# Kernel optimization log

Hardware: AMD Instinct MI355X
Metric: run time of the kernel (lower is better)

## Reference

```python
import jax, jax.numpy as jnp
import numpy as np
import math

B, L, D, H, FF = 2, 2048, 1024, 16, 4096
FACTOR = 5
EPS = 1e-5


def _ln(x, g, b):
    mu = jnp.mean(x, axis=-1, keepdims=True)
    var = jnp.mean((x - mu) ** 2, axis=-1, keepdims=True)
    return (x - mu) * jax.lax.rsqrt(var + EPS) * g + b


def setup_inputs() -> dict:
    key = jax.random.key(0)
    ks = jax.random.split(key, 16)
    s = D ** -0.5
    sample_k = min(FACTOR * int(np.ceil(np.log(L))), L)  # 40
    return {
        "x": jax.random.normal(ks[0], (B, L, D), jnp.float32),
        "Wq": jax.random.normal(ks[1], (D, D), jnp.float32) * s,
        "bq": jnp.zeros((D,), jnp.float32),
        "Wk": jax.random.normal(ks[2], (D, D), jnp.float32) * s,
        "bk": jnp.zeros((D,), jnp.float32),
        "Wv": jax.random.normal(ks[3], (D, D), jnp.float32) * s,
        "bv": jnp.zeros((D,), jnp.float32),
        "Wo": jax.random.normal(ks[4], (D, D), jnp.float32) * s,
        "bo": jnp.zeros((D,), jnp.float32),
        "ln1_g": jnp.ones((D,), jnp.float32),
        "ln1_b": jnp.zeros((D,), jnp.float32),
        "W1": jax.random.normal(ks[5], (D, FF), jnp.float32) * s,
        "b1": jnp.zeros((FF,), jnp.float32),
        "W2": jax.random.normal(ks[6], (FF, D), jnp.float32) * (FF ** -0.5),
        "b2": jnp.zeros((D,), jnp.float32),
        "ln2_g": jnp.ones((D,), jnp.float32),
        "ln2_b": jnp.zeros((D,), jnp.float32),
        "index_sample": jax.random.randint(ks[7], (L, sample_k), 0, L),
    }


def _prob_attn(Q, K, V, index_sample):
    # Q,K,V: [B,H,L,Dh]; Informer ProbAttention with mask_flag=True (causal).
    b, h, l, dh = Q.shape
    n_top = min(FACTOR * int(np.ceil(np.log(l))), l)
    # sampled scores: Q[l] . K[index_sample[l, s]]
    K_s = K[:, :, index_sample]                                  # [B,H,L,S,Dh]
    QKs = jnp.einsum("bhld,bhlsd->bhls", Q, K_s)                 # [B,H,L,S]
    M = QKs.max(-1) - QKs.sum(-1) / l                             # sparsity measure
    _, M_top = jax.lax.top_k(M, n_top)                            # [B,H,u]
    Q_red = jnp.take_along_axis(Q, M_top[..., None], axis=2)      # [B,H,u,Dh]
    scale = 1.0 / jnp.sqrt(jnp.asarray(dh, jnp.float32))
    scores = jnp.einsum("bhud,bhld->bhul", Q_red, K) * scale      # [B,H,u,L]
    causal = jnp.arange(l)[None, None, None, :] > M_top[..., None]
    scores = jnp.where(causal, -jnp.inf, scores)
    attn = jax.nn.softmax(scores, axis=-1)
    upd = jnp.einsum("bhul,bhld->bhud", attn, V)                  # [B,H,u,Dh]
    # initial context for masked case: running cumsum of V
    context = jnp.cumsum(V, axis=2)
    bi = jnp.arange(b)[:, None, None]
    hi = jnp.arange(h)[None, :, None]
    context = context.at[bi, hi, M_top].set(upd)
    return context                                               # [B,H,L,Dh]


def reference(x, Wq, bq, Wk, bk, Wv, bv, Wo, bo, ln1_g, ln1_b,
              W1, b1, W2, b2, ln2_g, ln2_b, index_sample):
    b, l, d = x.shape
    dh = d // H
    Q = (x @ Wq + bq).reshape(b, l, H, dh).transpose(0, 2, 1, 3)
    K = (x @ Wk + bk).reshape(b, l, H, dh).transpose(0, 2, 1, 3)
    V = (x @ Wv + bv).reshape(b, l, H, dh).transpose(0, 2, 1, 3)
    ctx = _prob_attn(Q, K, V, index_sample)
    ctx = ctx.transpose(0, 2, 1, 3).reshape(b, l, d)
    attn_out = ctx @ Wo + bo
    x1 = _ln(x + attn_out, ln1_g, ln1_b)
    ff = jnp.maximum(x1 @ W1 + b1, 0.0) @ W2 + b2
    return _ln(x1 + ff, ln2_g, ln2_b)
```

## Files before the change

### kernel.cpp

```cpp
#include <hip/hip_runtime.h>
#include <hip/hip_bf16.h>
#include <hip/hip_fp16.h>
#include <math.h>

constexpr int B = 2, L = 2048, D = 1024, H = 16, DH = 64, FFD = 4096;
constexpr int S = 40;
constexpr int U = 40;
constexpr float EPS = 1e-5f;
constexpr int NCHUNK = 32;
constexpr int CHLEN = L / NCHUNK;
constexpr int LD3 = 3 * D;
constexpr int LD2 = 2 * D;
constexpr int LDA2 = 2 * D;
constexpr int JT = 128;
constexpr int NJC = L / JT;

typedef __attribute__((ext_vector_type(8))) short short8;
typedef __attribute__((ext_vector_type(8))) _Float16 half8;
typedef __attribute__((ext_vector_type(4))) float f32x4;

__device__ __forceinline__ unsigned short f2bf(float v) {
  __hip_bfloat16 h = __float2bfloat16(v);
  return __builtin_bit_cast(unsigned short, h);
}
__device__ __forceinline__ float bf2f(unsigned short u) {
  unsigned int x = ((unsigned int)u) << 16;
  return __builtin_bit_cast(float, x);
}
__device__ __forceinline__ unsigned short f2h(float v) {
  __half h = __float2half(v);
  return __builtin_bit_cast(unsigned short, h);
}
__device__ __forceinline__ float h2f(unsigned short u) {
  return __half2float(__builtin_bit_cast(__half, u));
}

__device__ __forceinline__ void gload16(const void* g, void* l) {
  __builtin_amdgcn_global_load_lds(
      (const __attribute__((address_space(1))) void*)g,
      (__attribute__((address_space(3))) void*)l, 16, 0, 0);
}

template<int GBN, int MINB, bool RELU, bool OUT_BF16, bool F16, bool DUPA>
__global__ __launch_bounds__(256, MINB) void gemm_kernel(
    const unsigned short* __restrict__ A,
    const unsigned short* __restrict__ Bt,
    const float* __restrict__ bias,
    const float* __restrict__ biasB,
    void* __restrict__ C, int M, int N, int K, int KA) {
  constexpr int GBM = 128, GBK = 64;
  constexpr int ABUF = GBM * GBK;
  constexpr int BBUF = GBN * GBK;
  constexpr int BUFS = ABUF + BBUF;
  constexpr int NI = GBN / 32;
  constexpr int NLOADS = 4 + GBN / 32;
  __shared__ short lds[2 * BUFS];

  const int tid  = threadIdx.x;
  const int lane = tid & 63;
  const int wid  = tid >> 6;
  const int wr = wid >> 1;
  const int wc = wid & 1;

  const int nwg  = gridDim.x * gridDim.y;
  const int orig = blockIdx.y * gridDim.x + blockIdx.x;
  const int wg   = (orig & 7) * (nwg >> 3) + (orig >> 3);
  const int bm = (wg / gridDim.x) * GBM;
  const int bn = (wg % gridDim.x) * GBN;

  const int srow  = lane >> 3;
  const int sslot = (lane & 7) ^ srow;
  const unsigned short* aS = A  + (size_t)(bm + wid * 8 + srow) * KA + sslot * 8;
  const unsigned short* bS = Bt + (size_t)(bn + wid * 8 + srow) * K  + sslot * 8;
  short* la0 = lds + wid * 8 * GBK;
  short* lb0 = lds + ABUF + wid * 8 * GBK;

  auto STAGE = [&](int buf, int kt) {
    const int akt = (DUPA && kt >= 16) ? kt - 16 : kt;
    const unsigned short* ap = aS + (size_t)akt * GBK;
    const unsigned short* bp = bS + (size_t)kt  * GBK;
    short* la = la0 + buf * BUFS;
    short* lb = lb0 + buf * BUFS;
    gload16(ap,                   la);
    gload16(ap + (size_t)32 * KA, la + 32 * GBK);
    gload16(ap + (size_t)64 * KA, la + 64 * GBK);
    gload16(ap + (size_t)96 * KA, la + 96 * GBK);
    #pragma unroll
    for (int r = 0; r < GBN / 32; ++r)
      gload16(bp + (size_t)(r * 32) * K, lb + r * 32 * GBK);
  };

  const int fr = lane & 15, g = lane >> 4;
  const int nt = K / GBK;

  STAGE(0, 0);

  f32x4 acc[4][NI] = {};
  int cur = 0;
  for (int t = 0; t < nt; ++t) {
    const int kt = (t + 1 < nt) ? t + 1 : t;
    STAGE(cur ^ 1, kt);
    if constexpr (NLOADS == 8)
      asm volatile("s_waitcnt vmcnt(8)" ::: "memory");
    else
      asm volatile("s_waitcnt vmcnt(6)" ::: "memory");
    __builtin_amdgcn_sched_barrier(0);
    __builtin_amdgcn_s_barrier();

    const short* la = lds + cur * BUFS;
    const short* lb = la + ABUF;
    short8 av[2][4], bv[2][NI];
    #pragma unroll
    for (int kk = 0; kk < 2; ++kk) {
      #pragma unroll
      for (int mi = 0; mi < 4; ++mi) {
        const int row = wr * 64 + mi * 16 + fr;
        av[kk][mi] = *(const short8*)&la[row * GBK + ((((kk << 2) | g) ^ (fr & 7)) << 3)];
      }
      #pragma unroll
      for (int ni = 0; ni < NI; ++ni) {
        const int row = wc * (GBN / 2) + ni * 16 + fr;
        bv[kk][ni] = *(const short8*)&lb[row * GBK + ((((kk << 2) | g) ^ (fr & 7)) << 3)];
      }
    }
    __builtin_amdgcn_s_setprio(1);
    #pragma unroll
    for (int kk = 0; kk < 2; ++kk)
      #pragma unroll
      for (int mi = 0; mi < 4; ++mi)
        #pragma unroll
        for (int ni = 0; ni < NI; ++ni) {
          if constexpr (F16)
            acc[mi][ni] = __builtin_amdgcn_mfma_f32_16x16x32_f16(
                __builtin_bit_cast(half8, av[kk][mi]),
                __builtin_bit_cast(half8, bv[kk][ni]), acc[mi][ni], 0, 0, 0);
          else
            acc[mi][ni] = __builtin_amdgcn_mfma_f32_16x16x32_bf16(
                av[kk][mi], bv[kk][ni], acc[mi][ni], 0, 0, 0);
        }
    __builtin_amdgcn_s_setprio(0);
    asm volatile("s_waitcnt lgkmcnt(0)" ::: "memory");
    __builtin_amdgcn_sched_barrier(0);
    __builtin_amdgcn_s_barrier();
    cur ^= 1;
  }

  #pragma unroll
  for (int ni = 0; ni < NI; ++ni) {
    const int col = bn + wc * (GBN / 2) + ni * 16 + fr;
    const float bcol = DUPA ? (col < D ? bias[col] : biasB[col - D]) : bias[col];
    #pragma unroll
    for (int mi = 0; mi < 4; ++mi) {
      #pragma unroll
      for (int j = 0; j < 4; ++j) {
        const int rowg = bm + wr * 64 + mi * 16 + (g << 2) + j;
        float v = acc[mi][ni][j] + bcol;
        if (RELU) v = fmaxf(v, 0.f);
        if (OUT_BF16) ((unsigned short*)C)[(size_t)rowg * N + col] = f2bf(v);
        else          ((float*)C)[(size_t)rowg * N + col] = v;
      }
    }
  }
}

__global__ __launch_bounds__(512, 1) void gemm_ff1_8ph_kernel(
    const unsigned short* __restrict__ A,
    const unsigned short* __restrict__ Bt,
    const float* __restrict__ bias,
    unsigned short* __restrict__ C, int M, int N, int K) {
  constexpr int BK = 64;
  __shared__ short lds8[2 * 32768];

  const int tid  = threadIdx.x;
  const int lane = tid & 63;
  const int wid  = tid >> 6;
  const int wrm  = wid >> 2;
  const int wcn  = wid & 3;

  const int nwg  = gridDim.x * gridDim.y;
  const int orig = blockIdx.y * gridDim.x + blockIdx.x;
  const int wg   = (orig & 7) * (nwg >> 3) + (orig >> 3);
  const int bm = (wg / gridDim.x) * 256;
  const int bn = (wg % gridDim.x) * 256;

  const int srow  = lane >> 3;
  const int sslot = (lane & 7) ^ srow;
  const unsigned short* aS = A  + (size_t)(bm + wid * 8 + srow) * K + sslot * 8;
  const unsigned short* bS = Bt + (size_t)(bn + wid * 8 + srow) * K + sslot * 8;
  short* ldsA0 = lds8 + wid * 8 * BK;
  short* ldsB0 = lds8 + 16384 + wid * 8 * BK;

  auto STAGE2 = [&](int buf, int kt, int part) {
    if (part < 2) {
      const unsigned short* ap = aS + (size_t)kt * BK;
      short* la = ldsA0 + buf * 32768;
      const int r0 = part * 128;
      gload16(ap + (size_t)r0 * K,        la + r0 * BK);
      gload16(ap + (size_t)(r0 + 64) * K, la + (r0 + 64) * BK);
    } else {
      const unsigned short* bp = bS + (size_t)kt * BK;
      short* lb = ldsB0 + buf * 32768;
      const int r0 = (part - 2) * 128;
      gload16(bp + (size_t)r0 * K,        lb + r0 * BK);
      gload16(bp + (size_t)(r0 + 64) * K, lb + (r0 + 64) * BK);
    }
  };

  const int fr = lane & 15, g = lane >> 4;
  const int nt = K / BK;

  #pragma unroll
  for (int p = 0; p < 4; ++p) STAGE2(0, 0, p);

  f32x4 acc[8][4] = {};
  short8 av[2][4], bv0[2][2], bv1[2][2];
  int bc = 0;
  for (int t = 0; t < nt; ++t) {
    const int kt = (t + 1 < nt) ? t + 1 : t;
    const short* la = lds8 + bc * 32768;
    const short* lb = la + 16384;

    STAGE2(bc ^ 1, kt, 0);
    asm volatile("s_waitcnt vmcnt(2)" ::: "memory");
    __builtin_amdgcn_sched_barrier(0);
    __builtin_amdgcn_s_barrier();

    #pragma unroll
    for (int kk = 0; kk < 2; ++kk) {
      #pragma unroll
      for (int mi = 0; mi < 4; ++mi) {
        const int row = wrm * 128 + mi * 16 + fr;
        av[kk][mi] = *(const short8*)&la[row * BK + ((((kk << 2) | g) ^ (fr & 7)) << 3)];
      }
      #pragma unroll
      for (int ni = 0; ni < 2; ++ni) {
        const int row = wcn * 64 + ni * 16 + fr;
        bv0[kk][ni] = *(const short8*)&lb[row * BK + ((((kk << 2) | g) ^ (fr & 7)) << 3)];
      }
    }
    asm volatile("s_waitcnt lgkmcnt(0)" ::: "memory");
    __builtin_amdgcn_sched_barrier(0);
    __builtin_amdgcn_s_setprio(1);
    #pragma unroll
    for (int kk = 0; kk < 2; ++kk)
      #pragma unroll
      for (int mi = 0; mi < 4; ++mi)
        #pragma unroll
        for (int ni = 0; ni < 2; ++ni)
          acc[mi][ni] = __builtin_amdgcn_mfma_f32_16x16x32_bf16(
              av[kk][mi], bv0[kk][ni], acc[mi][ni], 0, 0, 0);
    __builtin_amdgcn_s_setprio(0);

    STAGE2(bc ^ 1, kt, 1);
    #pragma unroll
    for (int kk = 0; kk < 2; ++kk)
      #pragma unroll
      for (int ni = 0; ni < 2; ++ni) {
        const int row = wcn * 64 + 32 + ni * 16 + fr;
        bv1[kk][ni] = *(const short8*)&lb[row * BK + ((((kk << 2) | g) ^ (fr & 7)) << 3)];
      }
    asm volatile("s_waitcnt lgkmcnt(0)" ::: "memory");
    __builtin_amdgcn_sched_barrier(0);
    __builtin_amdgcn_s_setprio(1);
    #pragma unroll
    for (int kk = 0; kk < 2; ++kk)
      #pragma unroll
      for (int mi = 0; mi < 4; ++mi)
        #pragma unroll
        for (int ni = 0; ni < 2; ++ni)
          acc[mi][2 + ni] = __builtin_amdgcn_mfma_f32_16x16x32_bf16(
              av[kk][mi], bv1[kk][ni], acc[mi][2 + ni], 0, 0, 0);
    __builtin_amdgcn_s_setprio(0);

    STAGE2(bc ^ 1, kt, 2);
    #pragma unroll
    for (int kk = 0; kk < 2; ++kk)
      #pragma unroll
      for (int mi = 0; mi < 4; ++mi) {
        const int row = wrm * 128 + 64 + mi * 16 + fr;
        av[kk][mi] = *(const short8*)&la[row * BK + ((((kk << 2) | g) ^ (fr & 7)) << 3)];
      }
    asm volatile("s_waitcnt lgkmcnt(0)" ::: "memory");
    __builtin_amdgcn_sched_barrier(0);
    __builtin_amdgcn_s_setprio(1);
    #pragma unroll
    for (int kk = 0; kk < 2; ++kk)
      #pragma unroll
      for (int mi = 0; mi < 4; ++mi)
        #pragma unroll
        for (int ni = 0; ni < 2; ++ni)
          acc[4 + mi][ni] = __builtin_amdgcn_mfma_f32_16x16x32_bf16(
              av[kk][mi], bv0[kk][ni], acc[4 + mi][ni], 0, 0, 0);
    __builtin_amdgcn_s_setprio(0);

    STAGE2(bc ^ 1, kt, 3);
    __builtin_amdgcn_s_setprio(1);
    #pragma unroll
    for (int kk = 0; kk < 2; ++kk)
      #pragma unroll
      for (int mi = 0; mi < 4; ++mi)
        #pragma unroll
        for (int ni = 0; ni < 2; ++ni)
          acc[4 + mi][2 + ni] = __builtin_amdgcn_mfma_f32_16x16x32_bf16(
              av[kk][mi], bv1[kk][ni], acc[4 + mi][2 + ni], 0, 0, 0);
    __builtin_amdgcn_s_setprio(0);
    __builtin_amdgcn_s_barrier();
    bc ^= 1;
  }

  #pragma unroll
  for (int NJ = 0; NJ < 4; ++NJ) {
    const int col = bn + wcn * 64 + NJ * 16 + fr;
    const float bcol = bias[col];
    #pragma unroll
    for (int MI = 0; MI < 8; ++MI) {
      #pragma unroll
      for (int j = 0; j < 4; ++j) {
        const int rowg = bm + wrm * 128 + MI * 16 + (g << 2) + j;
        float v = fmaxf(acc[MI][NJ][j] + bcol, 0.f);
        C[(size_t)rowg * N + col] = f2bf(v);
      }
    }
  }
}

__global__ __launch_bounds__(256) void prep_kernel(
    const float* __restrict__ x, unsigned short* __restrict__ A2,
    unsigned short* __restrict__ xb,
    const float* __restrict__ Wq, const float* __restrict__ Wk,
    unsigned short* __restrict__ B2r,
    const float* __restrict__ Wv, const float* __restrict__ Wo,
    const float* __restrict__ W1, const float* __restrict__ W2,
    unsigned short* __restrict__ Wvt, unsigned short* __restrict__ Wot,
    unsigned short* __restrict__ W1t, unsigned short* __restrict__ W2t) {
  const int bid = blockIdx.x;
  __shared__ float tile[32][33];
  if (bid < 4096) {
    const int i = (bid * 256 + threadIdx.x) * 4;
    const int m = i / D, k = i % D;
    const float4 v = *(const float4*)(x + i);
    ushort4 hi, lo, bb;
    hi.x = f2h(v.x); lo.x = f2h(v.x - h2f(hi.x)); bb.x = f2bf(v.x);
    hi.y = f2h(v.y); lo.y = f2h(v.y - h2f(hi.y)); bb.y = f2bf(v.y);
    hi.z = f2h(v.z); lo.z = f2h(v.z - h2f(hi.z)); bb.z = f2bf(v.z);
    hi.w = f2h(v.w); lo.w = f2h(v.w - h2f(hi.w)); bb.w = f2bf(v.w);
    unsigned short* row = A2 + (size_t)m * LDA2;
    *(ushort4*)(row + k)     = hi;
    *(ushort4*)(row + D + k) = lo;
    *(ushort4*)(xb + i) = bb;
    return;
  }
  const int tx = threadIdx.x & 31, ty = threadIdx.x >> 5;
  if (bid < 6144) {
    const int t = bid - 4096;
    const int z = t >> 10;
    const float* W = z ? Wk : Wq;
    unsigned short* outb = B2r + (size_t)z * D * LD3;
    const int bx = ((t & 1023) & 31) * 32;
    const int by = ((t & 1023) >> 5) * 32;
    #pragma unroll
    for (int i = ty; i < 32; i += 8)
      tile[i][tx] = W[(size_t)(by + i) * D + bx + tx];
    __syncthreads();
    #pragma unroll
    for (int i = ty; i < 32; i += 8) {
      const float v = tile[tx][i];
      const unsigned short hi = f2h(v);
      const unsigned short lo = f2h(v - h2f(hi));
      unsigned short* r = outb + (size_t)(bx + i) * LD3 + (by + tx);
      r[0]     = hi;
      r[D]     = lo;
      r[2 * D] = hi;
    }
    return;
  }
  const int tb = bid - 6144;
  const float* W; unsigned short* Wt; int K, N, t;
  if (tb < 1024)      { W = Wv; Wt = Wvt; K = D;   N = D;   t = tb; }
  else if (tb < 2048) { W = Wo; Wt = Wot; K = D;   N = D;   t = tb - 1024; }
  else if (tb < 6144) { W = W1; Wt = W1t; K = D;   N = FFD; t = tb - 2048; }
  else                { W = W2; Wt = W2t; K = FFD; N = D;   t = tb - 6144; }
  const int nx = N / 32;
  const int bx = (t % nx) * 32;
  const int by = (t / nx) * 32;
  #pragma unroll
  for (int i = ty; i < 32; i += 8)
    tile[i][tx] = W[(size_t)(by + i) * N + bx + tx];
  __syncthreads();
  #pragma unroll
  for (int i = ty; i < 32; i += 8)
    Wt[(size_t)(bx + i) * K + by + tx] = f2bf(tile[tx][i]);
}

__global__ __launch_bounds__(256) void prob_m_kernel(
    const float* __restrict__ QK, const int* __restrict__ idx,
    float* __restrict__ M_) {
  const int combo = blockIdx.x;
  const int b = combo >> 2, hg = combo & 3;
  const int l = blockIdx.y;
  const int tid = threadIdx.x;
  const int wave = tid >> 6;
  const int lane = tid & 63;
  const int h = hg * 4 + wave;
  __shared__ int sidx[S];
  if (tid < S) sidx[tid] = idx[l * S + tid];
  __syncthreads();
  const int dsub = (lane & 15) * 4;
  const int sgrp = lane >> 4;
  const float4 q = *(const float4*)(QK + ((size_t)b * L + l) * LD2 + h * DH + dsub);
  float mx = -INFINITY, sm = 0.f;
  for (int s = sgrp; s < S; s += 4) {
    const float4 kv = *(const float4*)(QK + ((size_t)b * L + sidx[s]) * LD2 + D + h * DH + dsub);
    float p = q.x*kv.x + q.y*kv.y + q.z*kv.z + q.w*kv.w;
    p += __shfl_xor(p, 1);
    p += __shfl_xor(p, 2);
    p += __shfl_xor(p, 4);
    p += __shfl_xor(p, 8);
    mx = fmaxf(mx, p);
    sm += p;
  }
  mx = fmaxf(mx, __shfl_xor(mx, 16));
  mx = fmaxf(mx, __shfl_xor(mx, 32));
  sm += __shfl_xor(sm, 16);
  sm += __shfl_xor(sm, 32);
  if (lane == 0)
    M_[((size_t)b * H + h) * L + l] = mx - sm / (float)L;
}

__global__ __launch_bounds__(64) void topk_kernel(
    const float* __restrict__ M_, int* __restrict__ Mtop) {
  const int bh = blockIdx.x;
  const float* row = M_ + (size_t)bh * L;
  const int lane = threadIdx.x;
  float v[32];
  #pragma unroll
  for (int k = 0; k < 32; ++k) v[k] = row[k * 64 + lane];
  for (int u = 0; u < U; ++u) {
    float best = v[0]; int bk = 0;
    #pragma unroll
    for (int k = 1; k < 32; ++k)
      if (v[k] > best) { best = v[k]; bk = k; }
    int bidx = bk * 64 + lane;
    #pragma unroll
    for (int off = 1; off < 64; off <<= 1) {
      const float ov = __shfl_xor(best, off);
      const int   oi = __shfl_xor(bidx, off);
      if (ov > best || (ov == best && oi < bidx)) { best = ov; bidx = oi; }
    }
    if (lane == 0) Mtop[bh * U + u] = bidx;
    if ((bidx & 63) == lane) {
      const int kk = bidx >> 6;
      #pragma unroll
      for (int k = 0; k < 32; ++k) if (k == kk) v[k] = -INFINITY;
    }
  }
}

__global__ __launch_bounds__(320) void attn_p1_kernel(
    const float* __restrict__ QK, const unsigned short* __restrict__ V16,
    const int* __restrict__ Mtop,
    float* __restrict__ pmax, float* __restrict__ psum, float* __restrict__ pv) {
  const int jc = blockIdx.x, h = blockIdx.y, b = blockIdx.z;
  const int bh = b * H + h;
  const int tid = threadIdx.x;
  const int j0 = jc * JT;
  __shared__ float Qs[U][68];
  __shared__ float KVs[JT][68];
  __shared__ unsigned short ws[U][JT];

  for (int i = tid; i < U * 16; i += 320) {
    const int u = i >> 4, dq = (i & 15) << 2;
    const int row = Mtop[bh * U + u];
    *(float4*)&Qs[u][dq] =
        *(const float4*)(QK + ((size_t)b * L + row) * LD2 + h * DH + dq);
  }
  for (int i = tid; i < JT * 16; i += 320) {
    const int j = i >> 4, dq = (i & 15) << 2;
    *(float4*)&KVs[j][dq] =
        *(const float4*)(QK + ((size_t)b * L + j0 + j) * LD2 + D + h * DH + dq);
  }
  __syncthreads();

  const int u = tid >> 3, jg = tid & 7;
  const int mt = Mtop[bh * U + u];
  float sc[16];
  #pragma unroll
  for (int jt = 0; jt < 16; ++jt) sc[jt] = 0.f;
  for (int dq = 0; dq < 64; dq += 4) {
    const float4 q = *(const float4*)&Qs[u][dq];
    #pragma unroll
    for (int jt = 0; jt < 16; ++jt) {
      const float4 k = *(const float4*)&KVs[jt * 8 + jg][dq];
      sc[jt] += q.x*k.x + q.y*k.y + q.z*k.z + q.w*k.w;
    }
  }
  float m = -INFINITY;
  #pragma unroll
  for (int jt = 0; jt < 16; ++jt) {
    const int j = j0 + jt * 8 + jg;
    sc[jt] = (j <= mt) ? sc[jt] * 0.125f : -INFINITY;
    m = fmaxf(m, sc[jt]);
  }
  m = fmaxf(m, __shfl_xor(m, 1));
  m = fmaxf(m, __shfl_xor(m, 2));
  m = fmaxf(m, __shfl_xor(m, 4));
  float sum = 0.f;
  #pragma unroll
  for (int jt = 0; jt < 16; ++jt) {
    const float e = (sc[jt] == -INFINITY) ? 0.f : expf(sc[jt] - m);
    sum += e;
    ws[u][jt * 8 + jg] = f2bf(e);
  }
  sum += __shfl_xor(sum, 1);
  sum += __shfl_xor(sum, 2);
  sum += __shfl_xor(sum, 4);
  if (jg == 0) {
    pmax[(size_t)(bh * NJC + jc) * U + u] = m;
    psum[(size_t)(bh * NJC + jc) * U + u] = sum;
  }
  __syncthreads();
  for (int i = tid; i < JT * 8; i += 320) {
    const int j = i >> 3, d8 = (i & 7) << 3;
    short8 vv = *(const short8*)(V16 + ((size_t)b * L + j0 + j) * D + h * DH + d8);
    #pragma unroll
    for (int e = 0; e < 8; ++e)
      KVs[j][d8 + e] = bf2f((unsigned short)vv[e]);
  }
  __syncthreads();
  const int d = tid & 63, ug = tid >> 6;
  float acc[8] = {};
  for (int j = 0; j < JT; j += 2) {
    const float v0 = KVs[j][d], v1 = KVs[j + 1][d];
    #pragma unroll
    for (int k = 0; k < 8; ++k) {
      const int uu = ug + k * 5;
      const unsigned int wp = *(const unsigned int*)&ws[uu][j];
      acc[k] = fmaf(bf2f((unsigned short)(wp & 0xffff)), v0, acc[k]);
      acc[k] = fmaf(bf2f((unsigned short)(wp >> 16)), v1, acc[k]);
    }
  }
  #pragma unroll
  for (int k = 0; k < 8; ++k) {
    const int uu = ug + k * 5;
    pv[((size_t)(bh * NJC + jc) * U + uu) * DH + d] = acc[k];
  }
}

__global__ __launch_bounds__(64) void attn_p2_kernel(
    const float* __restrict__ pmax, const float* __restrict__ psum,
    const float* __restrict__ pv, const int* __restrict__ Mtop,
    unsigned short* __restrict__ ctx16) {
  const int bid = blockIdx.x;
  const int u = bid % U, bh = bid / U;
  const int d = threadIdx.x;
  float gmax = -INFINITY;
  for (int c = 0; c < NJC; ++c)
    gmax = fmaxf(gmax, pmax[(size_t)(bh * NJC + c) * U + u]);
  float den = 0.f, num = 0.f;
  for (int c = 0; c < NJC; ++c) {
    const float m = pmax[(size_t)(bh * NJC + c) * U + u];
    if (m == -INFINITY) continue;
    const float s = expf(m - gmax);
    den += psum[(size_t)(bh * NJC + c) * U + u] * s;
    num += pv[((size_t)(bh * NJC + c) * U + u) * DH + d] * s;
  }
  const int h = bh % H, b = bh / H;
  const int l = Mtop[bh * U + u];
  ctx16[((size_t)b * L + l) * D + h * DH + d] = f2bf(num / den);
}

__global__ __launch_bounds__(256) void cumsum_pass1(
    const unsigned short* __restrict__ V16, float* __restrict__ csums) {
  const int cp = blockIdx.x * 256 + threadIdx.x;
  const int ch = blockIdx.y, b = blockIdx.z;
  size_t base = ((size_t)b * L + (size_t)ch * CHLEN) * D + cp * 2;
  float a0 = 0.f, a1 = 0.f;
  for (int i = 0; i < CHLEN; ++i) {
    const unsigned int u = *(const unsigned int*)(V16 + base + (size_t)i * D);
    a0 += bf2f((unsigned short)(u & 0xffff));
    a1 += bf2f((unsigned short)(u >> 16));
  }
  float* cs = csums + ((size_t)b * NCHUNK + ch) * D + cp * 2;
  cs[0] = a0; cs[1] = a1;
}

__global__ __launch_bounds__(256) void cumsum_pass2(
    const unsigned short* __restrict__ V16, const float* __restrict__ csums,
    unsigned short* __restrict__ ctx16) {
  const int cp = blockIdx.x * 256 + threadIdx.x;
  const int ch = blockIdx.y, b = blockIdx.z;
  float a0 = 0.f, a1 = 0.f;
  for (int j = 0; j < ch; ++j) {
    const float* cs = csums + ((size_t)b * NCHUNK + j) * D + cp * 2;
    a0 += cs[0]; a1 += cs[1];
  }
  size_t base = ((size_t)b * L + (size_t)ch * CHLEN) * D + cp * 2;
  for (int i = 0; i < CHLEN; ++i) {
    const size_t o = base + (size_t)i * D;
    const unsigned int u = *(const unsigned int*)(V16 + o);
    a0 += bf2f((unsigned short)(u & 0xffff));
    a1 += bf2f((unsigned short)(u >> 16));
    *(unsigned int*)(ctx16 + o) =
        (unsigned int)f2bf(a0) | ((unsigned int)f2bf(a1) << 16);
  }
}

template<bool ABF16>
__global__ __launch_bounds__(256) void add_ln_kernel(
    const void* __restrict__ a_, const unsigned short* __restrict__ r,
    const float* __restrict__ g, const float* __restrict__ be,
    float* __restrict__ out, unsigned short* __restrict__ out16) {
  const int row  = blockIdx.x * 4 + (threadIdx.x >> 6);
  const int lane = threadIdx.x & 63;
  float v[16];
  float s = 0.f;
  #pragma unroll
  for (int j = 0; j < 4; ++j) {
    const int c = j * 256 + lane * 4;
    float4 av;
    if (ABF16) {
      ushort4 ua = *(const ushort4*)((const unsigned short*)a_ + (size_t)row * D + c);
      av.x = bf2f(ua.x); av.y = bf2f(ua.y); av.z = bf2f(ua.z); av.w = bf2f(ua.w);
    } else {
      av = *(const float4*)((const float*)a_ + (size_t)row * D + c);
    }
    const ushort4 ur = *(const ushort4*)(r + (size_t)row * D + c);
    v[j*4+0] = av.x + bf2f(ur.x);
    v[j*4+1] = av.y + bf2f(ur.y);
    v[j*4+2] = av.z + bf2f(ur.z);
    v[j*4+3] = av.w + bf2f(ur.w);
    s += v[j*4+0] + v[j*4+1] + v[j*4+2] + v[j*4+3];
  }
  #pragma unroll
  for (int off = 1; off < 64; off <<= 1) s += __shfl_xor(s, off);
  const float mu = s / (float)D;
  float s2 = 0.f;
  #pragma unroll
  for (int k = 0; k < 16; ++k) { const float dv = v[k] - mu; s2 += dv * dv; }
  #pragma unroll
  for (int off = 1; off < 64; off <<= 1) s2 += __shfl_xor(s2, off);
  const float rstd = rsqrtf(s2 / (float)D + EPS);
  #pragma unroll
  for (int j = 0; j < 4; ++j) {
    const int c = j * 256 + lane * 4;
    const float4 gv = *(const float4*)(g + c);
    const float4 bv = *(const float4*)(be + c);
    float o0 = (v[j*4+0] - mu) * rstd * gv.x + bv.x;
    float o1 = (v[j*4+1] - mu) * rstd * gv.y + bv.y;
    float o2 = (v[j*4+2] - mu) * rstd * gv.z + bv.z;
    float o3 = (v[j*4+3] - mu) * rstd * gv.w + bv.w;
    if (out) {
      float4 ov; ov.x = o0; ov.y = o1; ov.z = o2; ov.w = o3;
      *(float4*)(out + (size_t)row * D + c) = ov;
    }
    if (out16) {
      ushort4 uo;
      uo.x = f2bf(o0); uo.y = f2bf(o1); uo.z = f2bf(o2); uo.w = f2bf(o3);
      *(ushort4*)(out16 + (size_t)row * D + c) = uo;
    }
  }
}

extern "C" void kernel_launch(void* const* d_in, const int* in_sizes, int n_in,
                              void* d_out, int out_size, void* d_ws, size_t ws_size,
                              hipStream_t stream) {
  const float* x   = (const float*)d_in[0];
  const float* Wq  = (const float*)d_in[1];
  const float* bq  = (const float*)d_in[2];
  const float* Wk  = (const float*)d_in[3];
  const float* bk  = (const float*)d_in[4];
  const float* Wv  = (const float*)d_in[5];
  const float* bv  = (const float*)d_in[6];
  const float* Wo  = (const float*)d_in[7];
  const float* bo  = (const float*)d_in[8];
  const float* g1  = (const float*)d_in[9];
  const float* be1 = (const float*)d_in[10];
  const float* W1  = (const float*)d_in[11];
  const float* b1  = (const float*)d_in[12];
  const float* W2  = (const float*)d_in[13];
  const float* b2  = (const float*)d_in[14];
  const float* g2  = (const float*)d_in[15];
  const float* be2 = (const float*)d_in[16];
  const int*   idx = (const int*)d_in[17];
  float* out = (float*)d_out;

  char* p = (char*)d_ws;
  unsigned short* A2     = (unsigned short*)p;
  unsigned short* AO16   = (unsigned short*)p;
  unsigned short* ff2_16 = (unsigned short*)(p + 8388608);
  unsigned short* xb    = (unsigned short*)(p + 16777216);
  unsigned short* ctx16 = (unsigned short*)(p + 16777216);
  unsigned short* B2 = (unsigned short*)(p + 25165824);
  char* scr = p + 25165824;
  float* Mbuf   = (float*)(scr);
  float* csum   = (float*)(scr + 262144);
  int*   Mtop   = (int*)  (scr + 524288);
  float* pmax   = (float*)(scr + 532480);
  float* psum   = (float*)(scr + 614400);
  float* pv     = (float*)(scr + 696320);
  float*          QKb = (float*)(p + 37748736);
  unsigned short* x1b = (unsigned short*)(p + 54525952);
  unsigned short* ff1b = (unsigned short*)(p + 62914560);
  unsigned short* Vb16 = (unsigned short*)(p + 96468992);
  unsigned short* Wvt = (unsigned short*)(p + 113246208);
  unsigned short* Wot = (unsigned short*)(p + 115343360);
  unsigned short* W1t = (unsigned short*)(p + 117440512);
  unsigned short* W2t = (unsigned short*)(p + 125829120);

  dim3 blk(256);
  const int M = B * L;

  prep_kernel<<<16384, blk, 0, stream>>>(x, A2, xb, Wq, Wk, B2,
                                         Wv, Wo, W1, W2, Wvt, Wot, W1t, W2t);
  gemm_kernel<128,2,false,false,true,true><<<dim3(LD2/128, M/128), blk, 0, stream>>>(
      A2, B2, bq, bk, QKb, M, LD2, LD3, LDA2);
  gemm_kernel<64,3,false,true,false,false><<<dim3(D/64, M/128), blk, 0, stream>>>(
      xb, Wvt, bv, bv, Vb16, M, D, D, D);
  prob_m_kernel<<<dim3(8, L), blk, 0, stream>>>(QKb, idx, Mbuf);
  topk_kernel<<<B*H, dim3(64), 0, stream>>>(Mbuf, Mtop);
  attn_p1_kernel<<<dim3(NJC, H, B), dim3(320), 0, stream>>>(QKb, Vb16, Mtop, pmax, psum, pv);
  cumsum_pass1<<<dim3(D/512, NCHUNK, B), blk, 0, stream>>>(Vb16, csum);
  cumsum_pass2<<<dim3(D/512, NCHUNK, B), blk, 0, stream>>>(Vb16, csum, ctx16);
  attn_p2_kernel<<<B*H*U, dim3(64), 0, stream>>>(pmax, psum, pv, Mtop, ctx16);
  gemm_kernel<64,3,false,true,false,false><<<dim3(D/64, M/128), blk, 0, stream>>>(
      ctx16, Wot, bo, bo, AO16, M, D, D, D);
  add_ln_kernel<false><<<B*L/4, blk, 0, stream>>>(x, AO16, g1, be1, nullptr, x1b);
  gemm_ff1_8ph_kernel<<<dim3(FFD/256, M/256), dim3(512), 0, stream>>>(
      x1b, W1t, b1, ff1b, M, FFD, D);
  gemm_kernel<64,3,false,true,false,false><<<dim3(D/64, M/128), blk, 0, stream>>>(
      ff1b, W2t, b2, b2, ff2_16, M, D, FFD, FFD);
  add_ln_kernel<true><<<B*L/4, blk, 0, stream>>>(x1b, ff2_16, g2, be2, out,
                                                 (unsigned short*)nullptr);
}
```

Before: 334.6 us.

## Add 8-wave pipelined QK projection GEMM with 256x128 tiles

Replaces the generic templated GEMM for the fused Q/K projection with a dedicated 512-thread kernel using 256x128 tiles, double-buffered LDS and global loads staged in three parts interleaved with MFMA phases. It also adds XCD-aware workgroup remapping and raises MFMA wave priority during compute. The aim is to hide global-load latency and improve data reuse for this GEMM. The cost is higher LDS and register use per workgroup and fewer workgroups in the grid.

```diff
diff --git a/kernel.cpp b/kernel.cpp
--- a/kernel.cpp
+++ b/kernel.cpp
@@ -158,6 +158,140 @@
         if (RELU) v = fmaxf(v, 0.f);
         if (OUT_BF16) ((unsigned short*)C)[(size_t)rowg * N + col] = f2bf(v);
         else          ((float*)C)[(size_t)rowg * N + col] = v;
+      }
+    }
+  }
+}
+
+__global__ __launch_bounds__(512, 1) void gemm_qk_8ph_kernel(
+    const unsigned short* __restrict__ A,
+    const unsigned short* __restrict__ Bt,
+    const float* __restrict__ bias,
+    const float* __restrict__ biasB,
+    float* __restrict__ C, int M, int N, int K, int KA) {
+  constexpr int BK = 64;
+  constexpr int ABUF = 256 * BK;
+  constexpr int BBUF = 128 * BK;
+  constexpr int BUFS = ABUF + BBUF;
+  __shared__ short lds[2 * BUFS];
+
+  const int tid  = threadIdx.x;
+  const int lane = tid & 63;
+  const int wid  = tid >> 6;
+  const int wrm  = wid >> 1;
+  const int wcn  = wid & 1;
+
+  const int nwg  = gridDim.x * gridDim.y;
+  const int orig = blockIdx.y * gridDim.x + blockIdx.x;
+  const int wg   = (orig & 7) * (nwg >> 3) + (orig >> 3);
+  const int bm = (wg / gridDim.x) * 256;
+  const int bn = (wg % gridDim.x) * 128;
+
+  const int srow  = lane >> 3;
+  const int sslot = (lane & 7) ^ srow;
+  const unsigned short* aS = A  + (size_t)(bm + wid * 8 + srow) * KA + sslot * 8;
+  const unsigned short* bS = Bt + (size_t)(bn + wid * 8 + srow) * K  + sslot * 8;
+  short* ldsA0 = lds + wid * 8 * BK;
+  short* ldsB0 = lds + ABUF + wid * 8 * BK;
+
+  auto STAGE2 = [&](int buf, int kt, int part) {
+    const int akt = (kt >= 16) ? kt - 16 : kt;
+    if (part < 2) {
+      const unsigned short* ap = aS + (size_t)akt * BK;
+      short* la = ldsA0 + buf * BUFS;
+      const int r0 = part * 128;
+      gload16(ap + (size_t)r0 * KA,        la + r0 * BK);
+      gload16(ap + (size_t)(r0 + 64) * KA, la + (r0 + 64) * BK);
+    } else {
+      const unsigned short* bp = bS + (size_t)kt * BK;
+      short* lb = ldsB0 + buf * BUFS;
+      gload16(bp,                  lb);
+      gload16(bp + (size_t)64 * K, lb + 64 * BK);
+    }
+  };
+
+  const int fr = lane & 15, g = lane >> 4;
+  const int nt = K / BK;
+
+  STAGE2(0, 0, 0); STAGE2(0, 0, 1); STAGE2(0, 0, 2);
+
+  f32x4 acc[4][4] = {};
+  short8 av[2][4], bv0[2][2], bv1[2][2];
+  int bc = 0;
+  for (int t = 0; t < nt; ++t) {
+    const int kt = (t + 1 < nt) ? t + 1 : t;
+    const short* la = lds + bc * BUFS;
+    const short* lb = la + ABUF;
+
+    STAGE2(bc ^ 1, kt, 0);
+    asm volatile("s_waitcnt vmcnt(2)" ::: "memory");
+    __builtin_amdgcn_sched_barrier(0);
+    __builtin_amdgcn_s_barrier();
+
+    #pragma unroll
+    for (int kk = 0; kk < 2; ++kk) {
+      #pragma unroll
+      for (int mi = 0; mi < 4; ++mi) {
+        const int row = wrm * 64 + mi * 16 + fr;
+        av[kk][mi] = *(const short8*)&la[row * BK + ((((kk << 2) | g) ^ (fr & 7)) << 3)];
+      }
+      #pragma unroll
+      for (int ni = 0; ni < 2; ++ni) {
+        const int row = wcn * 64 + ni * 16 + fr;
+        bv0[kk][ni] = *(const short8*)&lb[row * BK + ((((kk << 2) | g) ^ (fr & 7)) << 3)];
+      }
+    }
+    asm volatile("s_waitcnt lgkmcnt(0)" ::: "memory");
+    __builtin_amdgcn_sched_barrier(0);
+    __builtin_amdgcn_s_setprio(1);
+    #pragma unroll
+    for (int kk = 0; kk < 2; ++kk)
+      #pragma unroll
+      for (int mi = 0; mi < 4; ++mi)
+        #pragma unroll
+        for (int ni = 0; ni < 2; ++ni)
+          acc[mi][ni] = __builtin_amdgcn_mfma_f32_16x16x32_f16(
+              __builtin_bit_cast(half8, av[kk][mi]),
+              __builtin_bit_cast(half8, bv0[kk][ni]), acc[mi][ni], 0, 0, 0);
+    __builtin_amdgcn_s_setprio(0);
+
+    STAGE2(bc ^ 1, kt, 1);
+    #pragma unroll
+    for (int kk = 0; kk < 2; ++kk)
+      #pragma unroll
+      for (int ni = 0; ni < 2; ++ni) {
+        const int row = wcn * 64 + 32 + ni * 16 + fr;
+        bv1[kk][ni] = *(const short8*)&lb[row * BK + ((((kk << 2) | g) ^ (fr & 7)) << 3)];
+      }
+    asm volatile("s_waitcnt lgkmcnt(0)" ::: "memory");
+    __builtin_amdgcn_sched_barrier(0);
+    __builtin_amdgcn_s_setprio(1);
+    #pragma unroll
+    for (int kk = 0; kk < 2; ++kk)
+      #pragma unroll
+      for (int mi = 0; mi < 4; ++mi)
+        #pragma unroll
+        for (int ni = 0; ni < 2; ++ni)
+          acc[mi][2 + ni] = __builtin_amdgcn_mfma_f32_16x16x32_f16(
+              __builtin_bit_cast(half8, av[kk][mi]),
+              __builtin_bit_cast(half8, bv1[kk][ni]), acc[mi][2 + ni], 0, 0, 0);
+    __builtin_amdgcn_s_setprio(0);
+
+    STAGE2(bc ^ 1, kt, 2);
+    __builtin_amdgcn_s_barrier();
+    bc ^= 1;
+  }
+
+  #pragma unroll
+  for (int ni = 0; ni < 4; ++ni) {
+    const int col = bn + wcn * 64 + ni * 16 + fr;
+    const float bcol = (col < D) ? bias[col] : biasB[col - D];
+    #pragma unroll
+    for (int mi = 0; mi < 4; ++mi) {
+      #pragma unroll
+      for (int j = 0; j < 4; ++j) {
+        const int rowg = bm + wrm * 64 + mi * 16 + (g << 2) + j;
+        C[(size_t)rowg * N + col] = acc[mi][ni][j] + bcol;
       }
     }
   }
@@ -712,7 +846,7 @@
 
   prep_kernel<<<16384, blk, 0, stream>>>(x, A2, xb, Wq, Wk, B2,
                                          Wv, Wo, W1, W2, Wvt, Wot, W1t, W2t);
-  gemm_kernel<128,2,false,false,true,true><<<dim3(LD2/128, M/128), blk, 0, stream>>>(
+  gemm_qk_8ph_kernel<<<dim3(LD2/128, M/256), dim3(512), 0, stream>>>(
       A2, B2, bq, bk, QKb, M, LD2, LD3, LDA2);
   gemm_kernel<64,3,false,true,false,false><<<dim3(D/64, M/128), blk, 0, stream>>>(
       xb, Wvt, bv, bv, Vb16, M, D, D, D);
```

Result: slower. 342.4 us (+2.3%).
